# Optimization experiments

Hardware: AMD Instinct MI355X
Metric: run time of the kernel (lower is better)

## Reference

```python
import jax, jax.numpy as jnp
import numpy as np

BN_EPS = 1e-5


def conv2d(x, w, b, pad=1):
    # x: [B,Ci,H,W], w: [Co,Ci,kh,kw] (torch OIHW layout)
    y = jax.lax.conv_general_dilated(
        x, w, window_strides=(1, 1), padding=((pad, pad), (pad, pad)),
        dimension_numbers=("NCHW", "OIHW", "NCHW"))
    return y + b[None, :, None, None]


def conv_transpose2d(x, w, b):
    # torch ConvTranspose2d(k=3, stride=2, padding=1, output_padding=1)
    # w: [Ci, Co, 3, 3] (torch transpose-conv layout)
    # equivalent: lhs-dilated conv with flipped kernel, pad = (k-1-p, k-1-p+op) = (1, 2)
    wk = jnp.flip(w, axis=(2, 3)).transpose(1, 0, 2, 3)  # [Co, Ci, 3, 3]
    y = jax.lax.conv_general_dilated(
        x, wk, window_strides=(1, 1), padding=((1, 2), (1, 2)),
        lhs_dilation=(2, 2), dimension_numbers=("NCHW", "OIHW", "NCHW"))
    return y + b[None, :, None, None]


def setup_inputs() -> dict:
    key = jax.random.key(0)
    ks = jax.random.split(key, 10)
    B, Cin, Cout, E = 1024, 128, 64, 8
    s = lambda k, shape: jax.random.normal(k, shape, jnp.float32) * 0.05
    return {
        "x": jax.random.normal(ks[0], (B, Cin, 6, 6), jnp.float32),
        # gate params
        "gw": s(ks[1], (128, Cin, 3, 3)), "gb": jnp.zeros((128,), jnp.float32),
        "fc1_w": s(ks[2], (256, 128 * 9)), "fc1_b": jnp.zeros((256,), jnp.float32),
        "fc2_w": s(ks[3], (E, 256)), "fc2_b": jnp.zeros((E,), jnp.float32),
        # expert params, stacked over expert axis E (num_per_expert=1 block)
        "wd": s(ks[4], (E, Cin, Cout, 3, 3)), "bd": jnp.zeros((E, Cout), jnp.float32),
        "wc": s(ks[5], (E, Cout, Cout, 3, 3)), "bc": jnp.zeros((E, Cout), jnp.float32),
        # BatchNorm (inference / running stats)
        "bn_g": jnp.ones((E, Cout), jnp.float32),
        "bn_b": jnp.zeros((E, Cout), jnp.float32),
        "bn_m": s(ks[6], (E, Cout)),
        "bn_v": jax.random.uniform(ks[7], (E, Cout), jnp.float32, 0.5, 1.5),
        "top_k": 2,
    }


def reference(x, gw, gb, fc1_w, fc1_b, fc2_w, fc2_b,
              wd, bd, wc, bc, bn_g, bn_b, bn_m, bn_v, top_k):
    B = x.shape[0]

    # --- Gate: conv3x3 -> relu -> maxpool2x2 -> fc -> relu -> fc ---
    h = jax.nn.relu(conv2d(x, gw, gb))                       # [B,128,6,6]
    p = jax.lax.reduce_window(h, -jnp.inf, jax.lax.max,
                              (1, 1, 2, 2), (1, 1, 2, 2), "VALID")  # [B,128,3,3]
    z = jax.nn.relu(p.reshape(B, -1) @ fc1_w.T + fc1_b)
    logits = z @ fc2_w.T + fc2_b                             # [B,E]

    # --- All experts computed densely (as in source), vmapped over expert axis ---
    def expert(wd_e, bd_e, wc_e, bc_e, g_e, b_e, m_e, v_e):
        y = jax.nn.relu(conv_transpose2d(x, wd_e, bd_e))     # [B,Cout,12,12]
        y = conv2d(y, wc_e, bc_e)
        scale = (g_e * jax.lax.rsqrt(v_e + BN_EPS))[None, :, None, None]
        y = (y - m_e[None, :, None, None]) * scale + b_e[None, :, None, None]
        return jax.nn.relu(y)

    eo = jax.vmap(expert)(wd, bd, wc, bc, bn_g, bn_b, bn_m, bn_v)  # [E,B,C,12,12]

    # --- top-k routing: gather selected experts, softmax-weighted sum ---
    tw, ti = jax.lax.top_k(logits, top_k)                    # [B,k]
    tw = jax.nn.softmax(tw, axis=1)
    sel = jnp.take_along_axis(eo.transpose(1, 0, 2, 3, 4),
                              ti[:, :, None, None, None], axis=1)  # [B,k,C,12,12]
    return (sel * tw[:, :, None, None, None]).sum(axis=1)   # [B,C,12,12]
```

## Files before the change

### kernel.cpp

```cpp
#include <hip/hip_runtime.h>
#include <math.h>

typedef _Float16 f16x8 __attribute__((ext_vector_type(8)));
typedef float    f32x4 __attribute__((ext_vector_type(4)));

#define PWD_ELEMS 589824
#define PWC_ELEMS 294912
#define PWG_ELEMS 147456
#define PW1T_ELEMS 294912
#define WS_NEEDED_BYTES ((PWD_ELEMS + PWC_ELEMS + 2 * PWG_ELEMS) * 2 + 512 * 4 + 16384 + PW1T_ELEMS * 4)

__global__ void pack_weights(const float* __restrict__ wd,
                             const float* __restrict__ wc,
                             const float* __restrict__ gw,
                             const float* __restrict__ fc1_w,
                             const float* __restrict__ bc,
                             const float* __restrict__ bn_g,
                             const float* __restrict__ bn_b,
                             const float* __restrict__ bn_m,
                             const float* __restrict__ bn_v,
                             _Float16* __restrict__ pwd,
                             _Float16* __restrict__ pwc,
                             _Float16* __restrict__ pwg_hi,
                             _Float16* __restrict__ pwg_lo,
                             float* __restrict__ pbias,
                             float* __restrict__ pw1t)
{
  int i = blockIdx.x * 256 + threadIdx.x;
  if (i < PWD_ELEMS) {
    int j  = i & 7;
    int l  = (i >> 3) & 63;
    int nt = (i >> 9) & 3;
    int ks = (i >> 11) & 3;
    int rest = i >> 13;
    int t = rest % 9, e = rest / 9;
    int ky = t / 3, kx = t % 3;
    int k = ks * 32 + (l >> 4) * 8 + j;
    int n = nt * 16 + (l & 15);
    float v = wd[(((size_t)e * 128 + k) * 64 + n) * 9 + (2 - ky) * 3 + (2 - kx)];
    pwd[i] = (_Float16)v;
    return;
  }
  i -= PWD_ELEMS;
  if (i < PWC_ELEMS) {
    int j  = i & 7;
    int l  = (i >> 3) & 63;
    int nt = (i >> 9) & 3;
    int ks = (i >> 11) & 1;
    int rest = i >> 12;
    int t = rest % 9, e = rest / 9;
    int ky = t / 3, kx = t % 3;
    int k = ks * 32 + (l >> 4) * 8 + j;
    int n = nt * 16 + (l & 15);
    float scale = bn_g[e * 64 + n] * rsqrtf(bn_v[e * 64 + n] + 1e-5f);
    float v = wc[(((size_t)e * 64 + n) * 64 + k) * 9 + ky * 3 + kx] * scale;
    pwc[i] = (_Float16)v;
    return;
  }
  i -= PWC_ELEMS;
  if (i < PWG_ELEMS) {
    int j  = i & 7;
    int l  = (i >> 3) & 63;
    int nt = (i >> 9) & 7;
    int ks = (i >> 12) & 3;
    int t  = i >> 14;
    int ky = t / 3, kx = t % 3;
    int k = ks * 32 + (l >> 4) * 8 + j;
    int n = nt * 16 + (l & 15);
    float v = gw[(size_t)n * 1152 + k * 9 + ky * 3 + kx];
    _Float16 hi = (_Float16)v;
    pwg_hi[i] = hi;
    pwg_lo[i] = (_Float16)(v - (float)hi);
    return;
  }
  i -= PWG_ELEMS;
  if (i < 512) {
    int e = i >> 6, n = i & 63;
    float scale = bn_g[e * 64 + n] * rsqrtf(bn_v[e * 64 + n] + 1e-5f);
    pbias[i] = (bc[e * 64 + n] - bn_m[e * 64 + n]) * scale + bn_b[e * 64 + n];
    return;
  }
  i -= 512;
  if (i < PW1T_ELEMS) {
    int k = i >> 8, o = i & 255;
    pw1t[i] = fc1_w[(size_t)o * 1152 + k];
  }
}

__global__ __launch_bounds__(256, 2) void cmoe_gate(
    const float* __restrict__ x, const float* __restrict__ gb,
    const float* __restrict__ pw1t, const float* __restrict__ fc1_b,
    const float* __restrict__ fc2_w, const float* __restrict__ fc2_b,
    const _Float16* __restrict__ pwg_hi, const _Float16* __restrict__ pwg_lo,
    int* __restrict__ route_i, float* __restrict__ route_w)
{
  const int b2 = blockIdx.x;
  const int tid = threadIdx.x;

  __shared__ __align__(16) char smem[72256];
  _Float16* xg_hi = (_Float16*)smem;
  _Float16* xg_lo = (_Float16*)(smem + 34816);
  float* zred = (float*)(smem + 44032);
  float* slog = (float*)(smem + 54272);

  const int w    = tid >> 6;
  const int lane = tid & 63;
  const int lr   = lane & 15;
  const int lq   = lane >> 4;

  for (int idx = tid; idx < 2 * 8192; idx += 256) {
    int s  = idx >> 13;
    int r  = idx & 8191;
    int sp = r >> 7, ci = r & 127;
    int row = sp >> 3, col = sp & 7;
    float v = 0.f;
    if (row >= 1 && row <= 6 && col >= 1 && col <= 6)
      v = x[(size_t)(2 * b2 + s) * 4608 + ci * 36 + (row - 1) * 6 + (col - 1)];
    _Float16 hi = (_Float16)v;
    xg_hi[s * 8704 + sp * 136 + ci] = hi;
    xg_lo[s * 8704 + sp * 136 + ci] = (_Float16)(v - (float)hi);
  }
  __syncthreads();

  int gA[3];
#pragma unroll
  for (int i = 0; i < 3; ++i) {
    int p = i * 16 + lr; if (p >= 36) p = 0;
    int oy = p / 6, ox = p % 6;
    gA[i] = (oy * 8 + ox) * 136 + lq * 8;
  }

  {
    f32x4 Cg[2][3][2];
    {
      float b0 = gb[(2 * w) * 16 + lr];
      float b1 = gb[(2 * w + 1) * 16 + lr];
#pragma unroll
      for (int s = 0; s < 2; ++s)
#pragma unroll
        for (int i = 0; i < 3; ++i) {
          Cg[s][i][0] = {b0, b0, b0, b0};
          Cg[s][i][1] = {b1, b1, b1, b1};
        }
    }
    const _Float16* pgh = pwg_hi + lane * 8;
    const _Float16* pgl = pwg_lo + lane * 8;

    for (int t = 0; t < 9; ++t) {
      const int gtap = ((t / 3) * 8 + (t % 3)) * 136;
#pragma unroll
      for (int ks = 0; ks < 4; ++ks) {
        const int boff = ((t * 4 + ks) * 8 + 2 * w) * 512;
        f16x8 Bh0 = *(const f16x8*)(pgh + boff);
        f16x8 Bh1 = *(const f16x8*)(pgh + boff + 512);
        f16x8 Bl0 = *(const f16x8*)(pgl + boff);
        f16x8 Bl1 = *(const f16x8*)(pgl + boff + 512);
#pragma unroll
        for (int s = 0; s < 2; ++s)
#pragma unroll
          for (int i = 0; i < 3; ++i) {
            f16x8 Ah = *(const f16x8*)(xg_hi + s * 8704 + gA[i] + gtap + ks * 32);
            f16x8 Al = *(const f16x8*)(xg_lo + s * 8704 + gA[i] + gtap + ks * 32);
            Cg[s][i][0] = __builtin_amdgcn_mfma_f32_16x16x32_f16(Ah, Bh0, Cg[s][i][0], 0, 0, 0);
            Cg[s][i][1] = __builtin_amdgcn_mfma_f32_16x16x32_f16(Ah, Bh1, Cg[s][i][1], 0, 0, 0);
            Cg[s][i][0] = __builtin_amdgcn_mfma_f32_16x16x32_f16(Al, Bh0, Cg[s][i][0], 0, 0, 0);
            Cg[s][i][1] = __builtin_amdgcn_mfma_f32_16x16x32_f16(Al, Bh1, Cg[s][i][1], 0, 0, 0);
            Cg[s][i][0] = __builtin_amdgcn_mfma_f32_16x16x32_f16(Ah, Bl0, Cg[s][i][0], 0, 0, 0);
            Cg[s][i][1] = __builtin_amdgcn_mfma_f32_16x16x32_f16(Ah, Bl1, Cg[s][i][1], 0, 0, 0);
          }
      }
    }
    __syncthreads();
#pragma unroll
    for (int s = 0; s < 2; ++s) {
      float* hb = (float*)(smem + 34816 + s * 18432);
#pragma unroll
      for (int i = 0; i < 3; ++i)
#pragma unroll
        for (int nn = 0; nn < 2; ++nn) {
          const int co_ = (2 * w + nn) * 16 + lr;
#pragma unroll
          for (int j = 0; j < 4; ++j) {
            int pix = i * 16 + lq * 4 + j;
            if (pix < 36) hb[co_ * 36 + pix] = fmaxf(Cg[s][i][nn][j], 0.f);
          }
        }
    }
  }
  __syncthreads();

  {
    float pr[2][5];
#pragma unroll
    for (int r = 0; r < 5; ++r) {
      int i = tid + 256 * r;
      if (i < 1152) {
        int co_ = i / 9, q = i % 9, py = q / 3, px = q % 3;
#pragma unroll
        for (int s = 0; s < 2; ++s) {
          const float* hp = (const float*)(smem + 34816 + s * 18432)
                            + co_ * 36 + (2 * py) * 6 + 2 * px;
          pr[s][r] = fmaxf(fmaxf(hp[0], hp[1]), fmaxf(hp[6], hp[7]));
        }
      }
    }
    __syncthreads();
#pragma unroll
    for (int r = 0; r < 5; ++r) {
      int i = tid + 256 * r;
      if (i < 1152) {
        ((float*)(smem + 34816))[i] = pr[0][r];
        ((float*)(smem + 39424))[i] = pr[1][r];
      }
    }
  }
  __syncthreads();

  {
    const float* pw = pw1t + w * 256 + 4 * lane;
    const float* p0 = (const float*)(smem + 34816);
    const float* p1 = (const float*)(smem + 39424);
    f32x4 a0 = {0.f, 0.f, 0.f, 0.f}, a1 = {0.f, 0.f, 0.f, 0.f};
#pragma unroll 4
    for (int m = 0; m < 288; ++m) {
      float pv0 = p0[w + 4 * m];
      float pv1 = p1[w + 4 * m];
      f32x4 wv = *(const f32x4*)(pw + m * 1024);
      a0.x += wv.x * pv0; a0.y += wv.y * pv0; a0.z += wv.z * pv0; a0.w += wv.w * pv0;
      a1.x += wv.x * pv1; a1.y += wv.y * pv1; a1.z += wv.z * pv1; a1.w += wv.w * pv1;
    }
    *(f32x4*)&zred[(0 * 4 + w) * 256 + 4 * lane] = a0;
    *(f32x4*)&zred[(1 * 4 + w) * 256 + 4 * lane] = a1;
  }
  __syncthreads();
  float* z0 = (float*)(smem + 52224);
  float* z1 = (float*)(smem + 53248);
  {
    float fb = fc1_b[tid];
    z0[tid] = fmaxf(zred[tid] + zred[256 + tid] + zred[512 + tid] + zred[768 + tid] + fb, 0.f);
    z1[tid] = fmaxf(zred[1024 + tid] + zred[1280 + tid] + zred[1536 + tid] + zred[1792 + tid] + fb, 0.f);
  }
  __syncthreads();

  if (tid < 128) {
    int s = tid >> 6, l = tid & 63;
    int o = l >> 3, t8 = l & 7;
    const float* zz = s ? z1 : z0;
    const float* wr = fc2_w + o * 256;
    float acc = 0.f;
    for (int k = t8; k < 256; k += 8) acc += zz[k] * wr[k];
    acc += __shfl_xor(acc, 1);
    acc += __shfl_xor(acc, 2);
    acc += __shfl_xor(acc, 4);
    if (t8 == 0) slog[s * 8 + o] = acc + fc2_b[o];
  }
  __syncthreads();

  if (tid == 0) {
#pragma unroll
    for (int s = 0; s < 2; ++s) {
      const float* sl = slog + s * 8;
      int i0 = 0; float v0 = sl[0];
#pragma unroll
      for (int o = 1; o < 8; ++o) { float v = sl[o]; if (v > v0) { v0 = v; i0 = o; } }
      int i1 = (i0 == 0) ? 1 : 0; float v1 = sl[i1];
#pragma unroll
      for (int o = 0; o < 8; ++o) {
        if (o != i0) { float v = sl[o]; if (v > v1) { v1 = v; i1 = o; } }
      }
      float e1 = expf(v1 - v0);
      float inv = 1.f / (1.f + e1);
      int sb = 2 * b2 + s;
      route_i[2 * sb] = i0; route_i[2 * sb + 1] = i1;
      route_w[2 * sb] = inv; route_w[2 * sb + 1] = e1 * inv;
    }
  }
}

#define ZOFF  4896
#define Y1OFF 5024

#define DECONV_TAP(KY, KX)                                                  \
  {                                                                         \
    constexpr int t_  = (KY) * 3 + (KX);                                    \
    constexpr int dy_ = ((KY) == 2) ? 1 : 0;                                \
    constexpr int dx_ = ((KX) == 2) ? 1 : 0;                                \
    int u0 = uA[0] + dy_, v0 = vA[0] + dx_;                                 \
    int u1 = uA[1] + dy_, v1 = vA[1] + dx_;                                 \
    int u2 = uA[2] + dy_, v2 = vA[2] + dx_;                                 \
    int b0_ = (pvA[0] && u0 < 6 && v0 < 6) ? (u0 * 6 + v0) * 136 : ZOFF;    \
    int b1_ = (pvA[1] && u1 < 6 && v1 < 6) ? (u1 * 6 + v1) * 136 : ZOFF;    \
    int b2_ = (pvA[2] && u2 < 6 && v2 < 6) ? (u2 * 6 + v2) * 136 : ZOFF;    \
    _Pragma("unroll")                                                       \
    for (int ks = 0; ks < 4; ++ks) {                                        \
      f16x8 Bf = *(const f16x8*)(pwd_e + (size_t)(t_ * 4 + ks) * 2048);     \
      f16x8 A0 = *(const f16x8*)(S + b0_ + lq * 8 + ks * 32);               \
      f16x8 A1 = *(const f16x8*)(S + b1_ + lq * 8 + ks * 32);               \
      f16x8 A2 = *(const f16x8*)(S + b2_ + lq * 8 + ks * 32);               \
      Cd0 = __builtin_amdgcn_mfma_f32_16x16x32_f16(A0, Bf, Cd0, 0, 0, 0);   \
      Cd1 = __builtin_amdgcn_mfma_f32_16x16x32_f16(A1, Bf, Cd1, 0, 0, 0);   \
      Cd2 = __builtin_amdgcn_mfma_f32_16x16x32_f16(A2, Bf, Cd2, 0, 0, 0);   \
    }                                                                       \
  }

#define STORE_CLASS(QY, QX)                                                 \
  _Pragma("unroll")                                                         \
  for (int i = 0; i < 3; ++i) {                                             \
    f32x4 Cv = (i == 0) ? Cd0 : ((i == 1) ? Cd1 : Cd2);                     \
    _Pragma("unroll")                                                       \
    for (int j = 0; j < 4; ++j) {                                           \
      int p = i * 16 + lq * 4 + j;                                          \
      if (p < 36) {                                                         \
        int u = p / 6, v = p - 6 * (p / 6);                                 \
        int oy = 2 * u + (QY), ox = 2 * v + (QX);                           \
        S[Y1OFF + ((oy + 1) * 14 + (ox + 1)) * 72 + co] =                   \
            (_Float16)fmaxf(Cv[j], 0.f);                                    \
      }                                                                     \
    }                                                                       \
  }

__global__ __launch_bounds__(256, 4) void cmoe_expert(
    const float* __restrict__ x,
    const float* __restrict__ bd,
    const _Float16* __restrict__ pwd, const _Float16* __restrict__ pwc,
    const float* __restrict__ pbias,
    const int* __restrict__ route_i, const float* __restrict__ route_w,
    float* __restrict__ out)
{
  const int b = blockIdx.x;
  const int tid = threadIdx.x;

  __shared__ __align__(16) char smem[38272];
  _Float16* S = (_Float16*)smem;
  float* sout = (float*)(smem + 10048);

  const int w    = tid >> 6;
  const int lane = tid & 63;
  const int lr   = lane & 15;
  const int lq   = lane >> 4;

  const int e0 = route_i[2 * b], e1 = route_i[2 * b + 1];
  const float w0 = route_w[2 * b], w1 = route_w[2 * b + 1];

  const float* xb = x + (size_t)b * 4608;
  for (int idx = tid; idx < 4608; idx += 256) {
    int ci = idx / 36, pix = idx - ci * 36;
    S[pix * 136 + ci] = (_Float16)xb[idx];
  }
  if (tid < 128) S[ZOFF + tid] = (_Float16)0.f;
  for (int idx = tid; idx < 52 * 72; idx += 256) {
    int sp = idx / 72, ci = idx % 72;
    int row, col;
    if (sp < 14)      { row = 0;       col = sp; }
    else if (sp < 28) { row = 13;      col = sp - 14; }
    else if (sp < 40) { row = sp - 27; col = 0; }
    else              { row = sp - 39; col = 13; }
    S[Y1OFF + (row * 14 + col) * 72 + ci] = (_Float16)0.f;
  }

  const int co = w * 16 + lr;

  int uA[3], vA[3], pvA[3];
#pragma unroll
  for (int i = 0; i < 3; ++i) {
    int p = i * 16 + lr;
    pvA[i] = (p < 36);
    int pc = pvA[i] ? p : 0;
    uA[i] = pc / 6; vA[i] = pc - 6 * (pc / 6);
  }
  int cA[9];
#pragma unroll
  for (int mt = 0; mt < 9; ++mt) {
    int pix = mt * 16 + lr;
    int oy = pix / 12, ox = pix - 12 * (pix / 12);
    cA[mt] = Y1OFF + (oy * 14 + ox) * 72 + lq * 8;
  }

  f32x4 facc[9];
#pragma unroll
  for (int mt = 0; mt < 9; ++mt) facc[mt] = {0.f, 0.f, 0.f, 0.f};

#pragma unroll 1
  for (int s = 0; s < 2; ++s) {
    const int e = s ? e1 : e0;
    const float wgt = s ? w1 : w0;
    const float db = bd[e * 64 + co];
    const _Float16* pwd_e = pwd + (size_t)e * (9 * 4 * 4 * 512) + w * 512 + lane * 8;

    __syncthreads();

    {
      f32x4 Cd0 = {db, db, db, db}, Cd1 = Cd0, Cd2 = Cd0;
      DECONV_TAP(0, 0) DECONV_TAP(0, 2) DECONV_TAP(2, 0) DECONV_TAP(2, 2)
      STORE_CLASS(1, 1)
    }
    {
      f32x4 Cd0 = {db, db, db, db}, Cd1 = Cd0, Cd2 = Cd0;
      DECONV_TAP(0, 1) DECONV_TAP(2, 1)
      STORE_CLASS(1, 0)
    }
    {
      f32x4 Cd0 = {db, db, db, db}, Cd1 = Cd0, Cd2 = Cd0;
      DECONV_TAP(1, 0) DECONV_TAP(1, 2)
      STORE_CLASS(0, 1)
    }
    {
      f32x4 Cd0 = {db, db, db, db}, Cd1 = Cd0, Cd2 = Cd0;
      DECONV_TAP(1, 1)
      STORE_CLASS(0, 0)
    }
    __syncthreads();

    f32x4 Cc[9];
    {
      const float cb = pbias[e * 64 + co];
#pragma unroll
      for (int mt = 0; mt < 9; ++mt) Cc[mt] = {cb, cb, cb, cb};
    }
    const _Float16* pwc_e = pwc + (size_t)e * (9 * 2 * 4 * 512) + w * 512 + lane * 8;

#pragma unroll
    for (int t = 0; t < 9; ++t) {
      const int ky = t / 3, kx = t % 3;
      const int aoff = (ky * 14 + kx) * 72;
#pragma unroll
      for (int ks = 0; ks < 2; ++ks) {
        f16x8 Bf = *(const f16x8*)(pwc_e + (size_t)(t * 2 + ks) * 2048);
#pragma unroll
        for (int mt = 0; mt < 9; ++mt) {
          f16x8 Af = *(const f16x8*)(S + cA[mt] + aoff + ks * 32);
          Cc[mt] = __builtin_amdgcn_mfma_f32_16x16x32_f16(Af, Bf, Cc[mt], 0, 0, 0);
        }
      }
    }

#pragma unroll
    for (int mt = 0; mt < 9; ++mt)
#pragma unroll
      for (int j = 0; j < 4; ++j)
        facc[mt][j] += wgt * fmaxf(Cc[mt][j], 0.f);
  }

  float* ob = out + (size_t)b * 9216;
  __syncthreads();
#pragma unroll
  for (int mt = 0; mt < 9; ++mt)
#pragma unroll
    for (int j = 0; j < 4; ++j) {
      int pix = mt * 16 + lq * 4 + j;
      if (pix < 72) sout[pix * 65 + co] = facc[mt][j];
    }
  __syncthreads();
  for (int j2 = tid; j2 < 4608; j2 += 256) {
    int c2 = j2 / 72, px = j2 - 72 * c2;
    ob[c2 * 144 + px] = sout[px * 65 + c2];
  }
  __syncthreads();
#pragma unroll
  for (int mt = 0; mt < 9; ++mt)
#pragma unroll
    for (int j = 0; j < 4; ++j) {
      int pix = mt * 16 + lq * 4 + j;
      if (pix >= 72) sout[(pix - 72) * 65 + co] = facc[mt][j];
    }
  __syncthreads();
  for (int j2 = tid; j2 < 4608; j2 += 256) {
    int c2 = j2 / 72, px = j2 - 72 * c2;
    ob[c2 * 144 + 72 + px] = sout[px * 65 + c2];
  }
}


#define DECONV_TAPS(q, ky, r)                                              \
  _Pragma("unroll")                                                        \
  for (int ox = 0; ox < 12; ++ox) {                                        \
    _Pragma("unroll")                                                      \
    for (int kx = 0; kx < 3; ++kx) {                                       \
      const int ss = ox + kx - 1;                                          \
      if (ss >= 0 && ss <= 10 && (ss & 1) == 0)                            \
        dacc[q][ox] += xr[r][ss >> 1] * w9[8 - ((ky) * 3 + (kx))];         \
    }                                                                      \
  }

__global__ __launch_bounds__(256, 2) void cmoe_ref(
    const float* __restrict__ x,
    const float* __restrict__ gw, const float* __restrict__ gb,
    const float* __restrict__ fc1_w, const float* __restrict__ fc1_b,
    const float* __restrict__ fc2_w, const float* __restrict__ fc2_b,
    const float* __restrict__ wd, const float* __restrict__ bd,
    const float* __restrict__ wc, const float* __restrict__ bc,
    const float* __restrict__ bn_g, const float* __restrict__ bn_b,
    const float* __restrict__ bn_m, const float* __restrict__ bn_v,
    float* __restrict__ out)
{
  const int b = blockIdx.x;
  const int tid = threadIdx.x;

  __shared__ float sx[128 * 48];
  __shared__ float sbuf[64 * 168];
  __shared__ int   se[2];
  __shared__ float swv[2];

  const float* xb = x + (size_t)b * 4608;
  for (int i = tid; i < 4608; i += 256) {
    int ci = i / 36, rem = i % 36;
    sx[ci * 48 + 6 + rem] = xb[i];
  }
  for (int i = tid; i < 128 * 12; i += 256) {
    int ci = i / 12, j = i % 12;
    sx[ci * 48 + (j < 6 ? j : 36 + j)] = 0.f;
  }
  __syncthreads();

  {
    const int co = tid >> 1;
    const int hh = tid & 1;
    float hacc[3][6];
    const float bias = gb[co];
#pragma unroll
    for (int q = 0; q < 3; ++q)
#pragma unroll
      for (int ox = 0; ox < 6; ++ox) hacc[q][ox] = bias;

    const float* wbase = gw + co * 1152;
    const float* xsb = sx + hh * 18;
    for (int ci = 0; ci < 128; ++ci) {
      const float* wr = wbase + ci * 9;
      float w9[9];
#pragma unroll
      for (int k = 0; k < 9; ++k) w9[k] = wr[k];
      const float* xr = xsb + ci * 48;
#pragma unroll
      for (int s = 0; s < 5; ++s) {
        float r8[8];
        r8[0] = 0.f; r8[7] = 0.f;
#pragma unroll
        for (int c = 0; c < 6; ++c) r8[c + 1] = xr[s * 6 + c];
#pragma unroll
        for (int ky = 0; ky < 3; ++ky) {
          const int q = s - ky;
          if (q >= 0 && q < 3) {
#pragma unroll
            for (int ox = 0; ox < 6; ++ox)
#pragma unroll
              for (int kx = 0; kx < 3; ++kx)
                hacc[q][ox] += r8[ox + kx] * w9[ky * 3 + kx];
          }
        }
      }
    }
#pragma unroll
    for (int q = 0; q < 3; ++q)
#pragma unroll
      for (int ox = 0; ox < 6; ++ox)
        sbuf[co * 36 + (3 * hh + q) * 6 + ox] = fmaxf(hacc[q][ox], 0.f);
  }
  __syncthreads();

  {
    float* sp = sbuf + 4608;
    for (int i = tid; i < 1152; i += 256) {
      int co = i / 9, r = i % 9, py = r / 3, px = r % 3;
      const float* hp = sbuf + co * 36 + (2 * py) * 6 + 2 * px;
      sp[i] = fmaxf(fmaxf(hp[0], hp[1]), fmaxf(hp[6], hp[7]));
    }
  }
  __syncthreads();

  {
    const float* sp = sbuf + 4608;
    float* sz = sbuf + 5760;
    float acc = fc1_b[tid];
    const float4* wr = (const float4*)(fc1_w + (size_t)tid * 1152);
    const float4* p4 = (const float4*)sp;
#pragma unroll 4
    for (int k = 0; k < 288; ++k) {
      float4 wv4 = wr[k], pv = p4[k];
      acc += wv4.x * pv.x + wv4.y * pv.y + wv4.z * pv.z + wv4.w * pv.w;
    }
    sz[tid] = fmaxf(acc, 0.f);
  }
  __syncthreads();

  {
    const float* sz = sbuf + 5760;
    float* slog = sbuf + 6016;
    if (tid < 8) {
      float acc = fc2_b[tid];
      const float* wr = fc2_w + tid * 256;
      for (int k = 0; k < 256; ++k) acc += sz[k] * wr[k];
      slog[tid] = acc;
    }
  }
  __syncthreads();

  if (tid == 0) {
    const float* slog = sbuf + 6016;
    int i0 = 0; float v0 = slog[0];
#pragma unroll
    for (int o = 1; o < 8; ++o) { float v = slog[o]; if (v > v0) { v0 = v; i0 = o; } }
    int i1 = (i0 == 0) ? 1 : 0; float v1 = slog[i1];
#pragma unroll
    for (int o = 0; o < 8; ++o) {
      if (o != i0) { float v = slog[o]; if (v > v1) { v1 = v; i1 = o; } }
    }
    float e1 = expf(v1 - v0);
    float inv = 1.f / (1.f + e1);
    se[0] = i0; se[1] = i1; swv[0] = inv; swv[1] = e1 * inv;
  }
  __syncthreads();

  for (int i = tid; i < 64 * 24; i += 256) {
    int ci = i / 24, j = i % 24;
    sbuf[ci * 168 + (j < 12 ? j : 144 + j)] = 0.f;
  }

  const int wv = tid >> 6;
  const int co = tid & 63;
  const int iyb = (wv & 1) ? (3 * wv - 1) / 2 : (3 * wv) / 2;

  float facc[3][12];
#pragma unroll
  for (int q = 0; q < 3; ++q)
#pragma unroll
    for (int ox = 0; ox < 12; ++ox) facc[q][ox] = 0.f;

  for (int slot = 0; slot < 2; ++slot) {
    const int e = se[slot];
    const float wgt = swv[slot];

    float dacc[3][12];
    {
      const float db = bd[e * 64 + co];
#pragma unroll
      for (int q = 0; q < 3; ++q)
#pragma unroll
        for (int ox = 0; ox < 12; ++ox) dacc[q][ox] = db;

      const float* wdb = wd + ((size_t)e * 128 * 64 + co) * 9;
      for (int ci = 0; ci < 128; ++ci) {
        const float* wr = wdb + (size_t)ci * 576;
        float w9[9];
#pragma unroll
        for (int k = 0; k < 9; ++k) w9[k] = wr[k];
        float xr[3][6];
#pragma unroll
        for (int r = 0; r < 3; ++r)
#pragma unroll
          for (int c = 0; c < 6; ++c)
            xr[r][c] = sx[ci * 48 + (iyb + r + 1) * 6 + c];
        if (wv & 1) {
          DECONV_TAPS(0, 0, 0)
          DECONV_TAPS(0, 2, 1)
          DECONV_TAPS(1, 1, 1)
          DECONV_TAPS(2, 0, 1)
          DECONV_TAPS(2, 2, 2)
        } else {
          DECONV_TAPS(0, 1, 0)
          DECONV_TAPS(1, 0, 0)
          DECONV_TAPS(1, 2, 1)
          DECONV_TAPS(2, 1, 1)
        }
      }
    }

    __syncthreads();
#pragma unroll
    for (int q = 0; q < 3; ++q)
#pragma unroll
      for (int ox = 0; ox < 12; ++ox)
        sbuf[co * 168 + (3 * wv + q + 1) * 12 + ox] = fmaxf(dacc[q][ox], 0.f);
    __syncthreads();

    float cacc[3][12];
    const float cb = bc[e * 64 + co];
#pragma unroll
    for (int q = 0; q < 3; ++q)
#pragma unroll
      for (int ox = 0; ox < 12; ++ox) cacc[q][ox] = cb;

    const float* wcb = wc + ((size_t)e * 64 + co) * 576;
    for (int ci = 0; ci < 64; ++ci) {
      const float* wr = wcb + ci * 9;
      float w9[9];
#pragma unroll
      for (int k = 0; k < 9; ++k) w9[k] = wr[k];
#pragma unroll
      for (int s = 0; s < 5; ++s) {
        float r14[14];
        r14[0] = 0.f; r14[13] = 0.f;
#pragma unroll
        for (int c = 0; c < 12; ++c) r14[c + 1] = sbuf[ci * 168 + (3 * wv + s) * 12 + c];
#pragma unroll
        for (int ky = 0; ky < 3; ++ky) {
          const int q = s - ky;
          if (q >= 0 && q < 3) {
#pragma unroll
            for (int ox = 0; ox < 12; ++ox)
#pragma unroll
              for (int kx = 0; kx < 3; ++kx)
                cacc[q][ox] += r14[ox + kx] * w9[ky * 3 + kx];
          }
        }
      }
    }

    const float g = bn_g[e * 64 + co], bb = bn_b[e * 64 + co];
    const float mm = bn_m[e * 64 + co], vvv = bn_v[e * 64 + co];
    const float scale = g * rsqrtf(vvv + 1e-5f);
#pragma unroll
    for (int q = 0; q < 3; ++q)
#pragma unroll
      for (int ox = 0; ox < 12; ++ox) {
        float v = (cacc[q][ox] - mm) * scale + bb;
        facc[q][ox] += wgt * fmaxf(v, 0.f);
      }
  }

  float* ob = out + ((size_t)b * 64 + co) * 144;
#pragma unroll
  for (int q = 0; q < 3; ++q)
#pragma unroll
    for (int ox = 0; ox < 12; ++ox)
      ob[(3 * wv + q) * 12 + ox] = facc[q][ox];
}

extern "C" void kernel_launch(void* const* d_in, const int* in_sizes, int n_in,
                              void* d_out, int out_size, void* d_ws, size_t ws_size,
                              hipStream_t stream) {
  const float* x     = (const float*)d_in[0];
  const float* gw    = (const float*)d_in[1];
  const float* gb    = (const float*)d_in[2];
  const float* fc1_w = (const float*)d_in[3];
  const float* fc1_b = (const float*)d_in[4];
  const float* fc2_w = (const float*)d_in[5];
  const float* fc2_b = (const float*)d_in[6];
  const float* wd    = (const float*)d_in[7];
  const float* bd    = (const float*)d_in[8];
  const float* wc    = (const float*)d_in[9];
  const float* bc    = (const float*)d_in[10];
  const float* bn_g  = (const float*)d_in[11];
  const float* bn_b  = (const float*)d_in[12];
  const float* bn_m  = (const float*)d_in[13];
  const float* bn_v  = (const float*)d_in[14];
  float* out = (float*)d_out;

  if (ws_size >= (size_t)WS_NEEDED_BYTES && d_ws != nullptr) {
    _Float16* pwd    = (_Float16*)d_ws;
    _Float16* pwc    = pwd + PWD_ELEMS;
    _Float16* pwg_hi = pwc + PWC_ELEMS;
    _Float16* pwg_lo = pwg_hi + PWG_ELEMS;
    float*    pbias  = (float*)(pwg_lo + PWG_ELEMS);
    int*      route_i = (int*)(pbias + 512);
    float*    route_w = (float*)(route_i + 2048);
    float*    pw1t   = route_w + 2048;

    int total = PWD_ELEMS + PWC_ELEMS + PWG_ELEMS + 512 + PW1T_ELEMS;
    pack_weights<<<dim3((total + 255) / 256), dim3(256), 0, stream>>>(
        wd, wc, gw, fc1_w, bc, bn_g, bn_b, bn_m, bn_v,
        pwd, pwc, pwg_hi, pwg_lo, pbias, pw1t);
    cmoe_gate<<<dim3(512), dim3(256), 0, stream>>>(
        x, gb, pw1t, fc1_b, fc2_w, fc2_b, pwg_hi, pwg_lo, route_i, route_w);
    cmoe_expert<<<dim3(1024), dim3(256), 0, stream>>>(
        x, bd, pwd, pwc, pbias, route_i, route_w, out);
  } else {
    cmoe_ref<<<dim3(1024), dim3(256), 0, stream>>>(
        x, gw, gb, fc1_w, fc1_b, fc2_w, fc2_b,
        wd, bd, wc, bc, bn_g, bn_b, bn_m, bn_v, out);
  }
}
```

Before: 158.0 us.

## Pad LDS strides to cut bank conflicts and split conv2 into three M-groups

Widens the shared-memory row strides for the input tile (136→140 halves) and the deconv output tile (72→76 halves), which shifts bank mapping to reduce LDS bank conflicts on the f16x8 A-fragment loads. It also restructures the second conv so it runs as three passes of three M-tiles instead of one pass over all nine accumulators, lowering the number of live accumulator registers. The cost is that each conv weight fragment is now loaded three times from global/cache instead of once. The LDS footprint also grows slightly, which may affect occupancy.

```diff
diff --git a/kernel.cpp b/kernel.cpp
--- a/kernel.cpp
+++ b/kernel.cpp
@@ -277,8 +277,10 @@
   }
 }
 
-#define ZOFF  4896
-#define Y1OFF 5024
+#define XSTRH  140
+#define ZOFFH  5040
+#define Y1OFFH 5168
+#define Y1STR  76
 
 #define DECONV_TAP(KY, KX)                                                  \
   {                                                                         \
@@ -288,9 +290,9 @@
     int u0 = uA[0] + dy_, v0 = vA[0] + dx_;                                 \
     int u1 = uA[1] + dy_, v1 = vA[1] + dx_;                                 \
     int u2 = uA[2] + dy_, v2 = vA[2] + dx_;                                 \
-    int b0_ = (pvA[0] && u0 < 6 && v0 < 6) ? (u0 * 6 + v0) * 136 : ZOFF;    \
-    int b1_ = (pvA[1] && u1 < 6 && v1 < 6) ? (u1 * 6 + v1) * 136 : ZOFF;    \
-    int b2_ = (pvA[2] && u2 < 6 && v2 < 6) ? (u2 * 6 + v2) * 136 : ZOFF;    \
+    int b0_ = (pvA[0] && u0 < 6 && v0 < 6) ? (u0 * 6 + v0) * XSTRH : ZOFFH; \
+    int b1_ = (pvA[1] && u1 < 6 && v1 < 6) ? (u1 * 6 + v1) * XSTRH : ZOFFH; \
+    int b2_ = (pvA[2] && u2 < 6 && v2 < 6) ? (u2 * 6 + v2) * XSTRH : ZOFFH; \
     _Pragma("unroll")                                                       \
     for (int ks = 0; ks < 4; ++ks) {                                        \
       f16x8 Bf = *(const f16x8*)(pwd_e + (size_t)(t_ * 4 + ks) * 2048);     \
@@ -313,9 +315,34 @@
       if (p < 36) {                                                         \
         int u = p / 6, v = p - 6 * (p / 6);                                 \
         int oy = 2 * u + (QY), ox = 2 * v + (QX);                           \
-        S[Y1OFF + ((oy + 1) * 14 + (ox + 1)) * 72 + co] =                   \
+        S[Y1OFFH + ((oy + 1) * 14 + (ox + 1)) * Y1STR + co] =               \
             (_Float16)fmaxf(Cv[j], 0.f);                                    \
       }                                                                     \
+    }                                                                       \
+  }
+
+#define CONV2_G3(A0I, A1I, A2I, M0, M1, M2)                                 \
+  {                                                                         \
+    f32x4 Cc0 = {cb, cb, cb, cb}, Cc1 = Cc0, Cc2 = Cc0;                     \
+    _Pragma("unroll")                                                       \
+    for (int t = 0; t < 9; ++t) {                                           \
+      const int aoff = ((t / 3) * 14 + (t % 3)) * Y1STR;                    \
+      _Pragma("unroll")                                                     \
+      for (int ks = 0; ks < 2; ++ks) {                                      \
+        f16x8 Bf  = *(const f16x8*)(pwc_e + (size_t)(t * 2 + ks) * 2048);   \
+        f16x8 Af0 = *(const f16x8*)(S + (A0I) + aoff + ks * 32);            \
+        f16x8 Af1 = *(const f16x8*)(S + (A1I) + aoff + ks * 32);            \
+        f16x8 Af2 = *(const f16x8*)(S + (A2I) + aoff + ks * 32);            \
+        Cc0 = __builtin_amdgcn_mfma_f32_16x16x32_f16(Af0, Bf, Cc0, 0, 0, 0);\
+        Cc1 = __builtin_amdgcn_mfma_f32_16x16x32_f16(Af1, Bf, Cc1, 0, 0, 0);\
+        Cc2 = __builtin_amdgcn_mfma_f32_16x16x32_f16(Af2, Bf, Cc2, 0, 0, 0);\
+      }                                                                     \
+    }                                                                       \
+    _Pragma("unroll")                                                       \
+    for (int j = 0; j < 4; ++j) {                                           \
+      facc[M0][j] += wgt * fmaxf(Cc0[j], 0.f);                              \
+      facc[M1][j] += wgt * fmaxf(Cc1[j], 0.f);                              \
+      facc[M2][j] += wgt * fmaxf(Cc2[j], 0.f);                              \
     }                                                                       \
   }
 
@@ -330,9 +357,9 @@
   const int b = blockIdx.x;
   const int tid = threadIdx.x;
 
-  __shared__ __align__(16) char smem[38272];
+  __shared__ __align__(16) char smem[40128];
   _Float16* S = (_Float16*)smem;
-  float* sout = (float*)(smem + 10048);
+  float* sout = (float*)(smem + 2 * Y1OFFH);
 
   const int w    = tid >> 6;
   const int lane = tid & 63;
@@ -345,17 +372,17 @@
   const float* xb = x + (size_t)b * 4608;
   for (int idx = tid; idx < 4608; idx += 256) {
     int ci = idx / 36, pix = idx - ci * 36;
-    S[pix * 136 + ci] = (_Float16)xb[idx];
-  }
-  if (tid < 128) S[ZOFF + tid] = (_Float16)0.f;
-  for (int idx = tid; idx < 52 * 72; idx += 256) {
-    int sp = idx / 72, ci = idx % 72;
+    S[pix * XSTRH + ci] = (_Float16)xb[idx];
+  }
+  if (tid < 128) S[ZOFFH + tid] = (_Float16)0.f;
+  for (int idx = tid; idx < 52 * 64; idx += 256) {
+    int sp = idx >> 6, ci = idx & 63;
     int row, col;
     if (sp < 14)      { row = 0;       col = sp; }
     else if (sp < 28) { row = 13;      col = sp - 14; }
     else if (sp < 40) { row = sp - 27; col = 0; }
     else              { row = sp - 39; col = 13; }
-    S[Y1OFF + (row * 14 + col) * 72 + ci] = (_Float16)0.f;
+    S[Y1OFFH + (row * 14 + col) * Y1STR + ci] = (_Float16)0.f;
   }
 
   const int co = w * 16 + lr;
@@ -373,7 +400,7 @@
   for (int mt = 0; mt < 9; ++mt) {
     int pix = mt * 16 + lr;
     int oy = pix / 12, ox = pix - 12 * (pix / 12);
-    cA[mt] = Y1OFF + (oy * 14 + ox) * 72 + lq * 8;
+    cA[mt] = Y1OFFH + (oy * 14 + ox) * Y1STR + lq * 8;
   }
 
   f32x4 facc[9];
@@ -411,34 +438,11 @@
     }
     __syncthreads();
 
-    f32x4 Cc[9];
-    {
-      const float cb = pbias[e * 64 + co];
-#pragma unroll
-      for (int mt = 0; mt < 9; ++mt) Cc[mt] = {cb, cb, cb, cb};
-    }
+    const float cb = pbias[e * 64 + co];
     const _Float16* pwc_e = pwc + (size_t)e * (9 * 2 * 4 * 512) + w * 512 + lane * 8;
-
-#pragma unroll
-    for (int t = 0; t < 9; ++t) {
-      const int ky = t / 3, kx = t % 3;
-      const int aoff = (ky * 14 + kx) * 72;
-#pragma unroll
-      for (int ks = 0; ks < 2; ++ks) {
-        f16x8 Bf = *(const f16x8*)(pwc_e + (size_t)(t * 2 + ks) * 2048);
-#pragma unroll
-        for (int mt = 0; mt < 9; ++mt) {
-          f16x8 Af = *(const f16x8*)(S + cA[mt] + aoff + ks * 32);
-          Cc[mt] = __builtin_amdgcn_mfma_f32_16x16x32_f16(Af, Bf, Cc[mt], 0, 0, 0);
-        }
-      }
-    }
-
-#pragma unroll
-    for (int mt = 0; mt < 9; ++mt)
-#pragma unroll
-      for (int j = 0; j < 4; ++j)
-        facc[mt][j] += wgt * fmaxf(Cc[mt][j], 0.f);
+    CONV2_G3(cA[0], cA[1], cA[2], 0, 1, 2)
+    CONV2_G3(cA[3], cA[4], cA[5], 3, 4, 5)
+    CONV2_G3(cA[6], cA[7], cA[8], 6, 7, 8)
   }
 
   float* ob = out + (size_t)b * 9216;
```

Result: slower. 326.5 us (+106.7%).
